# Kernel optimization log

Hardware: AMD Instinct MI355X
Metric: run time of the kernel (lower is better)

## Reference

```python
import jax, jax.numpy as jnp
import numpy as np

N_SRC = 50000
N_DST = 50000
N_EDGES = 1_600_000
D_IN = 128
D_OUT = 128
NUM_HEADS = 8
SCALE = float((D_OUT // NUM_HEADS) ** 0.5)


def setup_inputs() -> dict:
    key = jax.random.key(0)
    ks = jax.random.split(key, 10)
    s = 1.0 / np.sqrt(D_IN)
    return {
        "src_feat": jax.random.normal(ks[0], (N_SRC, D_IN), dtype=jnp.float32),
        "dst_feat": jax.random.normal(ks[1], (N_DST, D_OUT), dtype=jnp.float32),
        "src_idx": jax.random.randint(ks[2], (N_EDGES,), 0, N_SRC, dtype=jnp.int64),
        "dst_idx": jax.random.randint(ks[3], (N_EDGES,), 0, N_DST, dtype=jnp.int64),
        "Wq": jax.random.normal(ks[4], (D_OUT, D_OUT), dtype=jnp.float32) * s,
        "bq": jnp.zeros((D_OUT,), dtype=jnp.float32),
        "Wk": jax.random.normal(ks[5], (D_OUT, D_IN), dtype=jnp.float32) * s,
        "bk": jnp.zeros((D_OUT,), dtype=jnp.float32),
        "Wv": jax.random.normal(ks[6], (D_OUT, D_IN), dtype=jnp.float32) * s,
        "bv": jnp.zeros((D_OUT,), dtype=jnp.float32),
    }


def reference(src_feat, dst_feat, src_idx, dst_idx, Wq, bq, Wk, bk, Wv, bv):
    # Node-level projections (torch Linear: x @ W.T + b)
    Q = dst_feat @ Wq.T + bq            # [N_dst, D_OUT]
    K = src_feat @ Wk.T + bk            # [N_src, D_OUT]
    V = src_feat @ Wv.T + bv            # [N_src, D_OUT]

    # Edge-wise full-dim dot-product score (heads only affect the scale)
    score = jnp.sum(Q[dst_idx] * K[src_idx], axis=-1) / SCALE  # [E]

    # Segment softmax over incoming edges of each destination node
    m = jax.ops.segment_max(score, dst_idx, num_segments=N_DST)   # [N_dst]
    e = jnp.exp(score - m[dst_idx])                               # [E]
    denom = jax.ops.segment_sum(e, dst_idx, num_segments=N_DST)   # [N_dst]
    attn = e / denom[dst_idx]                                     # [E]

    # Weighted V scatter-sum to destination nodes
    out = jax.ops.segment_sum(attn[:, None] * V[src_idx], dst_idx,
                              num_segments=N_DST)                 # [N_dst, D_OUT]
    return out
```

## Files before the change

### kernel.cpp

```cpp
#include <hip/hip_runtime.h>
#include <hip/hip_bf16.h>


#define D 128
#define E1 4096
#define BCAP 10240
#define LOG2E 1.44269504088896340736f

typedef __attribute__((ext_vector_type(8))) short bf16x8;
typedef __attribute__((ext_vector_type(4))) float f32x4;
typedef __attribute__((ext_vector_type(4))) int v4i;
typedef __attribute__((ext_vector_type(4))) unsigned v4u;

static __device__ __forceinline__ unsigned short f2bf(float f) {
  unsigned u = __float_as_uint(f);
  u += 0x7fff + ((u >> 16) & 1);
  return (unsigned short)(u >> 16);
}
static __device__ __forceinline__ float bfl(unsigned u) {
  return __uint_as_float(u << 16);
}
static __device__ __forceinline__ float bfh(unsigned u) {
  return __uint_as_float(u & 0xffff0000u);
}

template <int CTRL>
static __device__ __forceinline__ float dpp_add(float x) {
  int y = __builtin_amdgcn_update_dpp(0, __float_as_int(x), CTRL, 0xF, 0xF, false);
  return x + __int_as_float(y);
}

static __device__ __forceinline__ float dot8(const float4& qa, const float4& qb,
                                             const v4u k0, const v4u k1) {
  return (qa.x * bfl(k0.x) + qa.y * bfh(k0.x) + qa.z * bfl(k0.y) +
          qa.w * bfh(k0.y)) +
         (qb.x * bfl(k1.x) + qb.y * bfh(k1.x) + qb.z * bfl(k1.y) +
          qb.w * bfh(k1.y));
}

static __device__ __forceinline__ void stage_w(const float* __restrict__ W,
                                               char* lds) {
  const int tid = threadIdx.x;
#pragma unroll
  for (int i = 0; i < 8; ++i) {
    const int g = i * 256 + tid;
    const int r = g >> 4, c16 = g & 15;
    const float4 w0 = *(const float4*)(W + r * 128 + c16 * 8);
    const float4 w1 = *(const float4*)(W + r * 128 + c16 * 8 + 4);
    bf16x8 b;
    b[0] = f2bf(w0.x); b[1] = f2bf(w0.y); b[2] = f2bf(w0.z); b[3] = f2bf(w0.w);
    b[4] = f2bf(w1.x); b[5] = f2bf(w1.y); b[6] = f2bf(w1.z); b[7] = f2bf(w1.w);
    *(bf16x8*)(lds + r * 256 + (((c16 ^ (r & 7)) << 4))) = b;
  }
}

static __device__ __forceinline__ void stage_w_half(const float* __restrict__ W,
                                                    char* lds, int h) {
  const int tid = threadIdx.x;
#pragma unroll
  for (int i = 0; i < 4; ++i) {
    const int g = i * 256 + tid;
    const int r = g >> 4, c16 = g & 15;
    const float* wp = W + (size_t)(h * 64 + r) * 128 + c16 * 8;
    const float4 w0 = *(const float4*)(wp);
    const float4 w1 = *(const float4*)(wp + 4);
    bf16x8 b;
    b[0] = f2bf(w0.x); b[1] = f2bf(w0.y); b[2] = f2bf(w0.z); b[3] = f2bf(w0.w);
    b[4] = f2bf(w1.x); b[5] = f2bf(w1.y); b[6] = f2bf(w1.z); b[7] = f2bf(w1.w);
    *(bf16x8*)(lds + r * 256 + (((c16 ^ (r & 7)) << 4))) = b;
  }
}

static __device__ __forceinline__ bf16x8 ldw_lds(const char* lds, int n,
                                                 int colbyte) {
  return *(const bf16x8*)(lds + n * 256 + (colbyte ^ ((n & 7) << 4)));
}

static __device__ void bin1_body(
    int bx, int* h, int* basebuf, int* cur, const int* __restrict__ src_idx,
    const int* __restrict__ dst_idx, int* __restrict__ bins,
    int* __restrict__ bcount, int n) {
  const int tid = threadIdx.x;
  const int e0 = bx * E1;
  int dv[16], sv[16];
#pragma unroll
  for (int i = 0; i < 4; ++i) {
    int e = e0 + i * 1024 + tid * 4;
    if (e + 3 < n) {
      v4i d4 = __builtin_nontemporal_load((const v4i*)(dst_idx + e));
      v4i s4 = __builtin_nontemporal_load((const v4i*)(src_idx + e));
      dv[4 * i + 0] = d4.x; dv[4 * i + 1] = d4.y;
      dv[4 * i + 2] = d4.z; dv[4 * i + 3] = d4.w;
      sv[4 * i + 0] = s4.x; sv[4 * i + 1] = s4.y;
      sv[4 * i + 2] = s4.z; sv[4 * i + 3] = s4.w;
    } else {
      for (int k = 0; k < 4; ++k) {
        int ee = e + k;
        dv[4 * i + k] = (ee < n) ? dst_idx[ee] : -1;
        sv[4 * i + k] = (ee < n) ? src_idx[ee] : 0;
      }
    }
  }
  h[tid] = 0;
  __syncthreads();
#pragma unroll
  for (int i = 0; i < 16; ++i)
    if (dv[i] >= 0) atomicAdd(&h[dv[i] >> 8], 1);
  __syncthreads();
  const int c = h[tid];
  if (c > 0) basebuf[tid] = tid * BCAP + atomicAdd(&bcount[tid], c);
  cur[tid] = 0;
  __syncthreads();
#pragma unroll
  for (int i = 0; i < 16; ++i) {
    if (dv[i] >= 0) {
      const int b = dv[i] >> 8;
      const int r = atomicAdd(&cur[b], 1);
      const int off = basebuf[b] + r;
      if (off < (b + 1) * BCAP)
        bins[off] = sv[i] | ((dv[i] & 255) << 17);
    }
  }
}

static __device__ void bin2_body_1k(
    int b, int* smem, const int* __restrict__ bins,
    const int* __restrict__ bcount, int* __restrict__ csr,
    int* __restrict__ rowptr, int n_dst, int n_edges) {
  int* h = smem;
  int* ofs = smem + 256;
  int* cur = smem + 512;
  int* red = smem + 768;
  const int tid = threadIdx.x;

  if (tid < 256) red[tid] = (tid < b) ? min(bcount[tid], BCAP) : 0;
  __syncthreads();
  for (int off = 128; off > 0; off >>= 1) {
    if (tid < off) red[tid] += red[tid + off];
    __syncthreads();
  }
  const int gbase = red[0];
  const int cnt = min(bcount[b], BCAP);
  if (tid < 256) h[tid] = 0;
  __syncthreads();

  const int* bb = bins + b * BCAP;
  for (int i = tid; i < cnt; i += 1024) atomicAdd(&h[(bb[i] >> 17) & 255], 1);
  __syncthreads();

  const int myh = (tid < 256) ? h[tid] : 0;
  if (tid < 256) red[tid] = myh;
  __syncthreads();
  for (int off = 1; off < 256; off <<= 1) {
    int t = (tid >= off && tid < 256) ? red[tid - off] : 0;
    __syncthreads();
    if (tid < 256) red[tid] += t;
    __syncthreads();
  }
  if (tid < 256) {
    ofs[tid] = red[tid] - myh;
    cur[tid] = 0;
    const int d = b * 256 + tid;
    if (d < n_dst) rowptr[d] = gbase + ofs[tid];
    if (b == 0 && tid == 0) rowptr[n_dst] = n_edges;
  }
  __syncthreads();

  for (int i = tid; i < cnt; i += 1024) {
    const int p = bb[i];
    const int j = (p >> 17) & 255;
    const int r = atomicAdd(&cur[j], 1);
    csr[gbase + ofs[j] + r] = p & 0x1ffff;
  }
}

static __device__ void gemm_q_body(
    int bx, char* wlds, const float* __restrict__ X,
    const float* __restrict__ Wf, const float* __restrict__ bias,
    float* __restrict__ out, int N) {
  stage_w(Wf, wlds);
  __syncthreads();

  const int lane = threadIdx.x & 63;
  const int l15 = lane & 15, quad = lane >> 4;
  const int row0 = bx * 64 + (threadIdx.x >> 6) * 16;

  f32x4 acc[8];
#pragma unroll
  for (int t = 0; t < 8; ++t) acc[t] = (f32x4){0.f, 0.f, 0.f, 0.f};

  int ar = row0 + l15;
  if (ar >= N) ar = N - 1;
  const float* ap = X + (size_t)ar * D + quad * 8;

#pragma unroll
  for (int kc = 0; kc < 4; ++kc) {
    float4 a0 = *(const float4*)(ap + kc * 32);
    float4 a1 = *(const float4*)(ap + kc * 32 + 4);
    bf16x8 a;
    a[0] = f2bf(a0.x); a[1] = f2bf(a0.y); a[2] = f2bf(a0.z); a[3] = f2bf(a0.w);
    a[4] = f2bf(a1.x); a[5] = f2bf(a1.y); a[6] = f2bf(a1.z); a[7] = f2bf(a1.w);
    const int cb = kc * 64 + quad * 16;
#pragma unroll
    for (int t = 0; t < 8; ++t) {
      bf16x8 b = ldw_lds(wlds, t * 16 + l15, cb);
      acc[t] = __builtin_amdgcn_mfma_f32_16x16x32_bf16(a, b, acc[t], 0, 0, 0);
    }
  }
#pragma unroll
  for (int t = 0; t < 8; ++t) {
    const int c = t * 16 + l15;
    const float bc = bias[c];
#pragma unroll
    for (int r = 0; r < 4; ++r) {
      const int row = row0 + quad * 4 + r;
      if (row < N) out[(size_t)row * D + c] = acc[t][r] + bc;
    }
  }
}

static __device__ void gemm_kv_body(
    int bx, char* wlds, const float* __restrict__ X,
    const float* __restrict__ Wkf, const float* __restrict__ bk,
    const float* __restrict__ Wvf, const float* __restrict__ bv,
    unsigned short* __restrict__ KV, int N) {
  char* wk = wlds;
  char* wv = wlds + 16384;
  const int tid = threadIdx.x;
  const int lane = tid & 63;
  const int l15 = lane & 15, quad = lane >> 4;
  const int wave = tid >> 6;
  const int row0 = bx * 64 + wave * 16;

  int ar = row0 + l15;
  if (ar >= N) ar = N - 1;
  const float* ap = X + (size_t)ar * D + quad * 8;
  bf16x8 afrag[4];
#pragma unroll
  for (int kc = 0; kc < 4; ++kc) {
    float4 a0 = *(const float4*)(ap + kc * 32);
    float4 a1 = *(const float4*)(ap + kc * 32 + 4);
    afrag[kc][0] = f2bf(a0.x); afrag[kc][1] = f2bf(a0.y);
    afrag[kc][2] = f2bf(a0.z); afrag[kc][3] = f2bf(a0.w);
    afrag[kc][4] = f2bf(a1.x); afrag[kc][5] = f2bf(a1.y);
    afrag[kc][6] = f2bf(a1.z); afrag[kc][7] = f2bf(a1.w);
  }

  f32x4 accK[8], accV[8];
#pragma unroll
  for (int t = 0; t < 8; ++t) {
    accK[t] = (f32x4){0.f, 0.f, 0.f, 0.f};
    accV[t] = (f32x4){0.f, 0.f, 0.f, 0.f};
  }

#pragma unroll
  for (int h = 0; h < 2; ++h) {
    __syncthreads();
    stage_w_half(Wkf, wk, h);
    stage_w_half(Wvf, wv, h);
    __syncthreads();
#pragma unroll
    for (int kc = 0; kc < 4; ++kc) {
      const int cb = kc * 64 + quad * 16;
#pragma unroll
      for (int t = 0; t < 4; ++t) {
        const int n = t * 16 + l15;
        bf16x8 b0 = ldw_lds(wk, n, cb);
        bf16x8 b1 = ldw_lds(wv, n, cb);
        accK[h * 4 + t] =
            __builtin_amdgcn_mfma_f32_16x16x32_bf16(afrag[kc], b0,
                                                    accK[h * 4 + t], 0, 0, 0);
        accV[h * 4 + t] =
            __builtin_amdgcn_mfma_f32_16x16x32_bf16(afrag[kc], b1,
                                                    accV[h * 4 + t], 0, 0, 0);
      }
    }
  }

  __syncthreads();
  unsigned short (*stage)[256] = (unsigned short(*)[256])wlds;
#pragma unroll
  for (int t = 0; t < 8; ++t) {
    const int c = t * 16 + l15;
    const float bkc = bk[c], bvc = bv[c];
    const int ki = ((c >> 2) << 3) + (c & 3);
#pragma unroll
    for (int r = 0; r < 4; ++r) {
      const int lr = wave * 16 + quad * 4 + r;
      stage[lr][ki] = f2bf(accK[t][r] + bkc);
      stage[lr][ki + 4] = f2bf(accV[t][r] + bvc);
    }
  }
  __syncthreads();
  const int row_base = bx * 64;
#pragma unroll
  for (int i = 0; i < 8; ++i) {
    int idx = i * 256 + tid;
    int lr = idx >> 5;
    int c8 = (idx & 31) << 3;
    int grow = row_base + lr;
    if (grow < N)
      *(f32x4*)(KV + (size_t)grow * 256 + c8) = *(const f32x4*)&stage[lr][c8];
  }
}

static __device__ void fused_body(
    int v, const float* __restrict__ Q, const unsigned short* __restrict__ KV,
    const int* __restrict__ csr, const int* __restrict__ rowptr,
    float* __restrict__ out, int n_dst) {
  const int lane = threadIdx.x & 63;
  const int g = lane >> 4;
  const int gl = lane & 15;
  int d = v * 4 + (threadIdx.x >> 6);
  if (d >= n_dst) return;
  d = __builtin_amdgcn_readfirstlane(d);
  const int start = __builtin_amdgcn_readfirstlane(rowptr[d]);
  const int n = __builtin_amdgcn_readfirstlane(rowptr[d + 1]) - start;

  const float qs = 0.25f * LOG2E;
  float4 q0 = *(const float4*)(Q + (size_t)d * D + 4 * gl);
  float4 q1 = *(const float4*)(Q + (size_t)d * D + 64 + 4 * gl);
  q0.x *= qs; q0.y *= qs; q0.z *= qs; q0.w *= qs;
  q1.x *= qs; q1.y *= qs; q1.z *= qs; q1.w *= qs;

  f32x4 acc0 = (f32x4){0.f, 0.f, 0.f, 0.f};
  f32x4 acc1 = (f32x4){0.f, 0.f, 0.f, 0.f};
  float den = 0.f;
  const int* cp = csr + start;

  for (int base = 0; base < n; base += 64) {
    const int il = base + lane;
    const int iv = __builtin_nontemporal_load(cp + ((il < n) ? il : (n - 1)));
    const int m = min(64, n - base);
    for (int j = 0; j < m; j += 16) {
      const int s0 = __shfl(iv, j + g, 64);
      const int s1 = __shfl(iv, j + 4 + g, 64);
      const int s2 = __shfl(iv, j + 8 + g, 64);
      const int s3 = __shfl(iv, j + 12 + g, 64);
      const unsigned short* r0 = KV + (size_t)s0 * 256 + gl * 8;
      const unsigned short* r1 = KV + (size_t)s1 * 256 + gl * 8;
      const unsigned short* r2 = KV + (size_t)s2 * 256 + gl * 8;
      const unsigned short* r3 = KV + (size_t)s3 * 256 + gl * 8;
      const v4u a0 = *(const v4u*)(r0);
      const v4u a1 = *(const v4u*)(r0 + 128);
      const v4u b0 = *(const v4u*)(r1);
      const v4u b1 = *(const v4u*)(r1 + 128);
      const v4u c0 = *(const v4u*)(r2);
      const v4u c1 = *(const v4u*)(r2 + 128);
      const v4u e0 = *(const v4u*)(r3);
      const v4u e1 = *(const v4u*)(r3 + 128);

      float p0 = dot8(q0, q1, a0, a1);
      float p1 = dot8(q0, q1, b0, b1);
      float p2 = dot8(q0, q1, c0, c1);
      float p3 = dot8(q0, q1, e0, e1);

      p0 = dpp_add<0xB1>(p0);  p1 = dpp_add<0xB1>(p1);
      p2 = dpp_add<0xB1>(p2);  p3 = dpp_add<0xB1>(p3);
      p0 = dpp_add<0x4E>(p0);  p1 = dpp_add<0x4E>(p1);
      p2 = dpp_add<0x4E>(p2);  p3 = dpp_add<0x4E>(p3);
      p0 = dpp_add<0x141>(p0); p1 = dpp_add<0x141>(p1);
      p2 = dpp_add<0x141>(p2); p3 = dpp_add<0x141>(p3);
      p0 = dpp_add<0x140>(p0); p1 = dpp_add<0x140>(p1);
      p2 = dpp_add<0x140>(p2); p3 = dpp_add<0x140>(p3);

      const float w0 = (j + g < m)      ? exp2f(p0) : 0.f;
      const float w1 = (j + 4 + g < m)  ? exp2f(p1) : 0.f;
      const float w2 = (j + 8 + g < m)  ? exp2f(p2) : 0.f;
      const float w3 = (j + 12 + g < m) ? exp2f(p3) : 0.f;

      acc0[0] += w0 * bfl(a0.z) + w1 * bfl(b0.z) + w2 * bfl(c0.z) + w3 * bfl(e0.z);
      acc0[1] += w0 * bfh(a0.z) + w1 * bfh(b0.z) + w2 * bfh(c0.z) + w3 * bfh(e0.z);
      acc0[2] += w0 * bfl(a0.w) + w1 * bfl(b0.w) + w2 * bfl(c0.w) + w3 * bfl(e0.w);
      acc0[3] += w0 * bfh(a0.w) + w1 * bfh(b0.w) + w2 * bfh(c0.w) + w3 * bfh(e0.w);
      acc1[0] += w0 * bfl(a1.z) + w1 * bfl(b1.z) + w2 * bfl(c1.z) + w3 * bfl(e1.z);
      acc1[1] += w0 * bfh(a1.z) + w1 * bfh(b1.z) + w2 * bfh(c1.z) + w3 * bfh(e1.z);
      acc1[2] += w0 * bfl(a1.w) + w1 * bfl(b1.w) + w2 * bfl(c1.w) + w3 * bfl(e1.w);
      acc1[3] += w0 * bfh(a1.w) + w1 * bfh(b1.w) + w2 * bfh(c1.w) + w3 * bfh(e1.w);
      den += (w0 + w1) + (w2 + w3);
    }
  }

#pragma unroll
  for (int msk = 16; msk <= 32; msk <<= 1) {
    acc0[0] += __shfl_xor(acc0[0], msk, 64);
    acc0[1] += __shfl_xor(acc0[1], msk, 64);
    acc0[2] += __shfl_xor(acc0[2], msk, 64);
    acc0[3] += __shfl_xor(acc0[3], msk, 64);
    acc1[0] += __shfl_xor(acc1[0], msk, 64);
    acc1[1] += __shfl_xor(acc1[1], msk, 64);
    acc1[2] += __shfl_xor(acc1[2], msk, 64);
    acc1[3] += __shfl_xor(acc1[3], msk, 64);
    den += __shfl_xor(den, msk, 64);
  }

  if (lane < 16) {
    const float r = (n > 0) ? 1.0f / den : 0.f;
    f32x4 o0 = (f32x4){acc0[0] * r, acc0[1] * r, acc0[2] * r, acc0[3] * r};
    f32x4 o1 = (f32x4){acc1[0] * r, acc1[1] * r, acc1[2] * r, acc1[3] * r};
    __builtin_nontemporal_store(o0, (f32x4*)(out + (size_t)d * D + 4 * gl));
    __builtin_nontemporal_store(o1,
                                (f32x4*)(out + (size_t)d * D + 64 + 4 * gl));
  }
}


__global__ __launch_bounds__(256) void front_kernel(
    const int* __restrict__ src_idx, const int* __restrict__ dst_idx,
    int* __restrict__ bins, int* __restrict__ bcount, int n_edges,
    const float* __restrict__ dst_feat, const float* __restrict__ Wq,
    const float* __restrict__ bq, float* __restrict__ Q, int n_dst,
    const float* __restrict__ src_feat, const float* __restrict__ Wk,
    const float* __restrict__ bk, const float* __restrict__ Wv,
    const float* __restrict__ bv, unsigned short* __restrict__ KV, int n_src,
    int g1, int gq) {
  __shared__ char wlds[32768];
  const int b = blockIdx.x;
  if (b < g1) {
    int* sh = (int*)wlds;
    bin1_body(b, sh, sh + 256, sh + 512, src_idx, dst_idx, bins, bcount,
              n_edges);
  } else if (b < g1 + gq) {
    gemm_q_body(b - g1, wlds, dst_feat, Wq, bq, Q, n_dst);
  } else {
    gemm_kv_body(b - g1 - gq, wlds, src_feat, Wk, bk, Wv, bv, KV, n_src);
  }
}

__global__ __launch_bounds__(1024) void bin2_kernel(
    const int* __restrict__ bins, const int* __restrict__ bcount,
    int* __restrict__ csr, int* __restrict__ rowptr, int n_dst, int n_edges) {
  __shared__ int sh[1024];
  bin2_body_1k(blockIdx.x, sh, bins, bcount, csr, rowptr, n_dst, n_edges);
}

__global__ __launch_bounds__(256) void fused_agg_kernel(
    const float* __restrict__ Q, const unsigned short* __restrict__ KV,
    const int* __restrict__ csr, const int* __restrict__ rowptr,
    float* __restrict__ out, int n_dst) {
  fused_body(blockIdx.x, Q, KV, csr, rowptr, out, n_dst);
}

extern "C" void kernel_launch(void* const* d_in, const int* in_sizes, int n_in,
                              void* d_out, int out_size, void* d_ws,
                              size_t ws_size, hipStream_t stream) {
  const float* src_feat = (const float*)d_in[0];
  const float* dst_feat = (const float*)d_in[1];
  const int* src_idx = (const int*)d_in[2];
  const int* dst_idx = (const int*)d_in[3];
  const float* Wq = (const float*)d_in[4];
  const float* bq = (const float*)d_in[5];
  const float* Wk = (const float*)d_in[6];
  const float* bk = (const float*)d_in[7];
  const float* Wv = (const float*)d_in[8];
  const float* bv = (const float*)d_in[9];

  const int n_src = in_sizes[0] / D;
  const int n_dst = in_sizes[1] / D;
  const int n_edges = in_sizes[2];
  const int nbk = (n_dst + 255) >> 8;

  float* out = (float*)d_out;

  float* Q = (float*)d_ws;
  unsigned short* KV = (unsigned short*)(Q + (size_t)n_dst * D);
  int* bcount = (int*)(KV + (size_t)n_src * 256);
  int* rowptr = bcount + 256;
  int* csr = rowptr + (n_dst + 1);
  int* bins = csr + n_edges;

  (void)hipMemsetAsync(bcount, 0, 256 * sizeof(int), stream);

  dim3 blk(256);
  const int g1 = (n_edges + E1 - 1) / E1;
  const int gq = (n_dst + 63) / 64;
  const int gkv = (n_src + 63) / 64;
  const int nf = (n_dst + 3) / 4;

  front_kernel<<<dim3(g1 + gq + gkv), blk, 0, stream>>>(
      src_idx, dst_idx, bins, bcount, n_edges, dst_feat, Wq, bq, Q, n_dst,
      src_feat, Wk, bk, Wv, bv, KV, n_src, g1, gq);

  bin2_kernel<<<dim3(nbk), dim3(1024), 0, stream>>>(bins, bcount, csr, rowptr,
                                                    n_dst, n_edges);

  fused_agg_kernel<<<dim3(nf), blk, 0, stream>>>(Q, KV, csr, rowptr, out,
                                                 n_dst);
}
```

Baseline: 265.2 us.

## Split front kernel into bin and projection kernels, split aggregation into halves

Splits the combined front kernel into a separate edge binning kernel and a projection GEMM kernel. The binning kernel now uses only 3 KB of shared memory, so more of its blocks can be resident at once. The aggregation kernel is launched as two half-grid kernels on the same stream. In the Q GEMM, the activation loads are issued before the weights are staged into LDS, so global latency overlaps with the staging. The extra launches add overhead, and since everything is on one stream the kernels still run in order.

Result: slower. 279.5 us (+5.4%).

```diff
diff --git a/kernel.cpp b/kernel.cpp
--- a/kernel.cpp
+++ b/kernel.cpp
@@ -178,28 +178,34 @@
     int bx, char* wlds, const float* __restrict__ X,
     const float* __restrict__ Wf, const float* __restrict__ bias,
     float* __restrict__ out, int N) {
-  stage_w(Wf, wlds);
-  __syncthreads();
-
   const int lane = threadIdx.x & 63;
   const int l15 = lane & 15, quad = lane >> 4;
   const int row0 = bx * 64 + (threadIdx.x >> 6) * 16;
 
-  f32x4 acc[8];
-#pragma unroll
-  for (int t = 0; t < 8; ++t) acc[t] = (f32x4){0.f, 0.f, 0.f, 0.f};
-
   int ar = row0 + l15;
   if (ar >= N) ar = N - 1;
   const float* ap = X + (size_t)ar * D + quad * 8;
-
+  float4 a0v[4], a1v[4];
 #pragma unroll
   for (int kc = 0; kc < 4; ++kc) {
-    float4 a0 = *(const float4*)(ap + kc * 32);
-    float4 a1 = *(const float4*)(ap + kc * 32 + 4);
+    a0v[kc] = *(const float4*)(ap + kc * 32);
+    a1v[kc] = *(const float4*)(ap + kc * 32 + 4);
+  }
+
+  stage_w(Wf, wlds);
+  __syncthreads();
+
+  f32x4 acc[8];
+#pragma unroll
+  for (int t = 0; t < 8; ++t) acc[t] = (f32x4){0.f, 0.f, 0.f, 0.f};
+
+#pragma unroll
+  for (int kc = 0; kc < 4; ++kc) {
     bf16x8 a;
-    a[0] = f2bf(a0.x); a[1] = f2bf(a0.y); a[2] = f2bf(a0.z); a[3] = f2bf(a0.w);
-    a[4] = f2bf(a1.x); a[5] = f2bf(a1.y); a[6] = f2bf(a1.z); a[7] = f2bf(a1.w);
+    a[0] = f2bf(a0v[kc].x); a[1] = f2bf(a0v[kc].y);
+    a[2] = f2bf(a0v[kc].z); a[3] = f2bf(a0v[kc].w);
+    a[4] = f2bf(a1v[kc].x); a[5] = f2bf(a1v[kc].y);
+    a[6] = f2bf(a1v[kc].z); a[7] = f2bf(a1v[kc].w);
     const int cb = kc * 64 + quad * 16;
 #pragma unroll
     for (int t = 0; t < 8; ++t) {
@@ -405,25 +411,27 @@
 }
 
 
-__global__ __launch_bounds__(256) void front_kernel(
+__global__ __launch_bounds__(256) void bin1_kernel(
     const int* __restrict__ src_idx, const int* __restrict__ dst_idx,
-    int* __restrict__ bins, int* __restrict__ bcount, int n_edges,
+    int* __restrict__ bins, int* __restrict__ bcount, int n_edges) {
+  __shared__ int sh[768];
+  bin1_body(blockIdx.x, sh, sh + 256, sh + 512, src_idx, dst_idx, bins, bcount,
+            n_edges);
+}
+
+__global__ __launch_bounds__(256) void proj_kernel(
     const float* __restrict__ dst_feat, const float* __restrict__ Wq,
     const float* __restrict__ bq, float* __restrict__ Q, int n_dst,
     const float* __restrict__ src_feat, const float* __restrict__ Wk,
     const float* __restrict__ bk, const float* __restrict__ Wv,
     const float* __restrict__ bv, unsigned short* __restrict__ KV, int n_src,
-    int g1, int gq) {
+    int gq) {
   __shared__ char wlds[32768];
   const int b = blockIdx.x;
-  if (b < g1) {
-    int* sh = (int*)wlds;
-    bin1_body(b, sh, sh + 256, sh + 512, src_idx, dst_idx, bins, bcount,
-              n_edges);
-  } else if (b < g1 + gq) {
-    gemm_q_body(b - g1, wlds, dst_feat, Wq, bq, Q, n_dst);
+  if (b < gq) {
+    gemm_q_body(b, wlds, dst_feat, Wq, bq, Q, n_dst);
   } else {
-    gemm_kv_body(b - g1 - gq, wlds, src_feat, Wk, bk, Wv, bv, KV, n_src);
+    gemm_kv_body(b - gq, wlds, src_feat, Wk, bk, Wv, bv, KV, n_src);
   }
 }
 
@@ -434,11 +442,17 @@
   bin2_body_1k(blockIdx.x, sh, bins, bcount, csr, rowptr, n_dst, n_edges);
 }
 
-__global__ __launch_bounds__(256) void fused_agg_kernel(
+__global__ __launch_bounds__(256) void fused_a_kernel(
     const float* __restrict__ Q, const unsigned short* __restrict__ KV,
     const int* __restrict__ csr, const int* __restrict__ rowptr,
-    float* __restrict__ out, int n_dst) {
-  fused_body(blockIdx.x, Q, KV, csr, rowptr, out, n_dst);
+    float* __restrict__ out, int n_dst, int voff) {
+  fused_body(blockIdx.x + voff, Q, KV, csr, rowptr, out, n_dst);
+}
+__global__ __launch_bounds__(256) void fused_b_kernel(
+    const float* __restrict__ Q, const unsigned short* __restrict__ KV,
+    const int* __restrict__ csr, const int* __restrict__ rowptr,
+    float* __restrict__ out, int n_dst, int voff) {
+  fused_body(blockIdx.x + voff, Q, KV, csr, rowptr, out, n_dst);
 }
 
 extern "C" void kernel_launch(void* const* d_in, const int* in_sizes, int n_in,
@@ -476,14 +490,19 @@
   const int gq = (n_dst + 63) / 64;
   const int gkv = (n_src + 63) / 64;
   const int nf = (n_dst + 3) / 4;
-
-  front_kernel<<<dim3(g1 + gq + gkv), blk, 0, stream>>>(
-      src_idx, dst_idx, bins, bcount, n_edges, dst_feat, Wq, bq, Q, n_dst,
-      src_feat, Wk, bk, Wv, bv, KV, n_src, g1, gq);
+  const int nfh = (nf + 1) / 2;
+
+  bin1_kernel<<<dim3(g1), blk, 0, stream>>>(src_idx, dst_idx, bins, bcount,
+                                            n_edges);
+
+  proj_kernel<<<dim3(gq + gkv), blk, 0, stream>>>(
+      dst_feat, Wq, bq, Q, n_dst, src_feat, Wk, bk, Wv, bv, KV, n_src, gq);
 
   bin2_kernel<<<dim3(nbk), dim3(1024), 0, stream>>>(bins, bcount, csr, rowptr,
                                                     n_dst, n_edges);
 
-  fused_agg_kernel<<<dim3(nf), blk, 0, stream>>>(Q, KV, csr, rowptr, out,
-                                                 n_dst);
-}
+  fused_a_kernel<<<dim3(nfh), blk, 0, stream>>>(Q, KV, csr, rowptr, out, n_dst,
+                                                0);
+  fused_b_kernel<<<dim3(nf - nfh), blk, 0, stream>>>(Q, KV, csr, rowptr, out,
+                                                     n_dst, nfh);
+}
```
